# Performance work log

Measured on AMD Instinct MI355X. Metric: run time of the kernel, lower is better.

Reference implementation:

```python
import jax, jax.numpy as jnp
import numpy as np


def squash(s, axis=-1):
    sq = jnp.sum(s * s, axis=axis, keepdims=True)
    return sq / (1.0 + sq) * s / (jnp.sqrt(sq) + 1e-8)


def setup_inputs() -> dict:
    key = jax.random.key(0)
    k1, k2 = jax.random.split(key)
    B, IN_CAPS, IN_DIM = 32, 2048, 16
    NUM_CAPS, CAPS_DIM = 32, 32
    x = jax.random.normal(k1, (B, IN_CAPS, IN_DIM), dtype=jnp.float32)
    W = 0.01 * jax.random.normal(k2, (NUM_CAPS, IN_CAPS, CAPS_DIM, IN_DIM), dtype=jnp.float32)
    return {"x": x, "W": W, "routing_steps": 3}


def reference(x, W, routing_steps):
    # u_hat[b, j, i, c] = W[j, i, c, d] @ x[b, i, d]
    u_hat = jnp.einsum('jicd,bid->bjic', W, x)
    du = jax.lax.stop_gradient(u_hat)  # routing uses detached predictions
    B, J, I, C = u_hat.shape
    b = jnp.zeros((B, J, I, 1), dtype=u_hat.dtype)
    for _ in range(routing_steps - 1):
        c = jax.nn.softmax(b, axis=1)                  # over output capsules j
        s = jnp.sum(c * du, axis=2)                    # [B, J, C]
        v = squash(s)
        b = b + jnp.einsum('bjic,bjc->bji', du, v)[..., None]
    c = jax.nn.softmax(b, axis=1)
    s = jnp.sum(c * u_hat, axis=2)
    v = squash(s)                                      # [B, J, C]
    return v
```

## Files before the change

kernel.cpp:

```cpp
#include <hip/hip_runtime.h>
#include <hip/hip_bf16.h>

#define B_SZ   32
#define I_CAPS 2048
#define J_CAPS 32
#define C_DIM  32
#define D_DIM  16

#define IT     8
#define TILES  8
#define SPLIT  32
#define ROW_STRIDE 40

__device__ inline unsigned short f2bf(float f) {
    union { __hip_bfloat16 h; unsigned short u; } cv;
    cv.h = __float2bfloat16(f);
    return cv.u;
}
__device__ inline float bf2f(unsigned int u16) {
    unsigned int x = (u16 & 0xffffu) << 16;
    union { unsigned int u; float f; } cv; cv.u = x;
    return cv.f;
}

__global__ __launch_bounds__(256) void uhat_kernel(const float* __restrict__ W,
                                                   const float* __restrict__ x,
                                                   unsigned short* __restrict__ u) {
    const int i = blockIdx.x;
    const int t = threadIdx.x;

    __shared__ float xs[B_SZ][D_DIM];
    if (t < 128) {
        const int b = t >> 2, k = t & 3;
        const float4 v = *reinterpret_cast<const float4*>(
            &x[((size_t)b * I_CAPS + i) * D_DIM + k * 4]);
        *reinterpret_cast<float4*>(&xs[b][k * 4]) = v;
    }
    __syncthreads();

    const int j  = t >> 3;
    const int c0 = (t & 7) * 4;

    const float* Wp = W + (((size_t)j * I_CAPS + i) * C_DIM + c0) * D_DIM;
    float4 w[4][4];
#pragma unroll
    for (int k = 0; k < 4; ++k)
#pragma unroll
        for (int d4 = 0; d4 < 4; ++d4)
            w[k][d4] = *reinterpret_cast<const float4*>(Wp + k * D_DIM + d4 * 4);

#pragma unroll 2
    for (int b = 0; b < B_SZ; ++b) {
        float a0 = 0.f, a1 = 0.f, a2 = 0.f, a3 = 0.f;
#pragma unroll
        for (int d4 = 0; d4 < 4; ++d4) {
            const float4 xv = *reinterpret_cast<const float4*>(&xs[b][d4 * 4]);
            a0 += w[0][d4].x * xv.x + w[0][d4].y * xv.y + w[0][d4].z * xv.z + w[0][d4].w * xv.w;
            a1 += w[1][d4].x * xv.x + w[1][d4].y * xv.y + w[1][d4].z * xv.z + w[1][d4].w * xv.w;
            a2 += w[2][d4].x * xv.x + w[2][d4].y * xv.y + w[2][d4].z * xv.z + w[2][d4].w * xv.w;
            a3 += w[3][d4].x * xv.x + w[3][d4].y * xv.y + w[3][d4].z * xv.z + w[3][d4].w * xv.w;
        }
        ushort4 o;
        o.x = f2bf(a0); o.y = f2bf(a1); o.z = f2bf(a2); o.w = f2bf(a3);
        *reinterpret_cast<ushort4*>(
            &u[(((size_t)b * I_CAPS + i) * J_CAPS + j) * C_DIM + c0]) = o;
    }
}

__global__ __launch_bounds__(256) void route_kernel(const unsigned short* __restrict__ u,
                                                    const float* __restrict__ V,
                                                    float* __restrict__ s) {
    const int b      = blockIdx.y;
    const int i_base = blockIdx.x * (IT * TILES);
    const int t      = threadIdx.x;

    __shared__ unsigned short us[IT * J_CAPS * ROW_STRIDE];
    __shared__ float Vs[J_CAPS * 33];
    __shared__ float cjs[IT * J_CAPS];

    for (int n = t; n < J_CAPS * C_DIM; n += 256) {
        const int j = n >> 5, c = n & 31;
        Vs[j * 33 + c] = V[((size_t)b * J_CAPS + j) * C_DIM + c];
    }

    const int jA = t & 31, iA = t >> 5;
    const int jB = t >> 3, c4 = (t & 7) * 4;

    float sacc0 = 0.f, sacc1 = 0.f, sacc2 = 0.f, sacc3 = 0.f;

    for (int tile = 0; tile < TILES; ++tile) {
        const int i0 = i_base + tile * IT;
        __syncthreads();

        {
            const uint4* gsrc = reinterpret_cast<const uint4*>(
                u + ((size_t)b * I_CAPS + i0) * J_CAPS * C_DIM);
#pragma unroll
            for (int k = 0; k < 4; ++k) {
                const int n  = t + k * 256;
                const int il = n >> 7, rem = n & 127, j = rem >> 2, q = rem & 3;
                *reinterpret_cast<uint4*>(
                    &us[(il * J_CAPS + j) * ROW_STRIDE + q * 8]) = gsrc[n];
            }
        }
        __syncthreads();

        {
            const unsigned short* row = &us[(iA * J_CAPS + jA) * ROW_STRIDE];
            float l = 0.f;
#pragma unroll
            for (int cq = 0; cq < 8; ++cq) {
                const uint2 pk = *reinterpret_cast<const uint2*>(row + cq * 4);
                const float* Vr = &Vs[jA * 33 + cq * 4];
                l += bf2f(pk.x) * Vr[0] + bf2f(pk.x >> 16) * Vr[1]
                   + bf2f(pk.y) * Vr[2] + bf2f(pk.y >> 16) * Vr[3];
            }
            float m = l;
#pragma unroll
            for (int msk = 16; msk >= 1; msk >>= 1) m = fmaxf(m, __shfl_xor(m, msk));
            const float e = __expf(l - m);
            float ssum = e;
#pragma unroll
            for (int msk = 16; msk >= 1; msk >>= 1) ssum += __shfl_xor(ssum, msk);
            cjs[iA * J_CAPS + jA] = e / ssum;
        }
        __syncthreads();

        {
#pragma unroll
            for (int il = 0; il < IT; ++il) {
                const float cj = cjs[il * J_CAPS + jB];
                const unsigned short* row = &us[(il * J_CAPS + jB) * ROW_STRIDE + c4];
                const uint2 pk = *reinterpret_cast<const uint2*>(row);
                sacc0 += cj * bf2f(pk.x);
                sacc1 += cj * bf2f(pk.x >> 16);
                sacc2 += cj * bf2f(pk.y);
                sacc3 += cj * bf2f(pk.y >> 16);
            }
        }
    }

    float* sp = &s[((size_t)b * J_CAPS + jB) * C_DIM + c4];
    atomicAdd(sp + 0, sacc0);
    atomicAdd(sp + 1, sacc1);
    atomicAdd(sp + 2, sacc2);
    atomicAdd(sp + 3, sacc3);
}

__global__ __launch_bounds__(256) void squash_kernel(float* __restrict__ s,
                                                     float* __restrict__ V,
                                                     float* __restrict__ out,
                                                     int final_pass) {
    const int t   = threadIdx.x;
    const int row = blockIdx.x * 8 + (t >> 5);
    const int c   = t & 31;
    const float sv = s[row * 32 + c];
    float sq = sv * sv;
#pragma unroll
    for (int msk = 16; msk >= 1; msk >>= 1) sq += __shfl_xor(sq, msk);
    const float scale = sq / ((1.f + sq) * (sqrtf(sq) + 1e-8f));
    const float v = sv * scale;
    if (final_pass) out[row * 32 + c] = v;
    else            V[row * 32 + c] += v;
    s[row * 32 + c] = 0.f;
}

extern "C" void kernel_launch(void* const* d_in, const int* in_sizes, int n_in,
                              void* d_out, int out_size, void* d_ws, size_t ws_size,
                              hipStream_t stream) {
    const float* x = (const float*)d_in[0];
    const float* W = (const float*)d_in[1];
    float* out = (float*)d_out;

    unsigned short* u = (unsigned short*)d_ws;
    float* s = (float*)((char*)d_ws + (size_t)B_SZ * I_CAPS * J_CAPS * C_DIM * 2);
    float* V = s + B_SZ * J_CAPS * C_DIM;

    hipMemsetAsync(s, 0, 2 * (size_t)B_SZ * J_CAPS * C_DIM * sizeof(float), stream);

    uhat_kernel<<<I_CAPS, 256, 0, stream>>>(W, x, u);

    for (int p = 0; p < 3; ++p) {
        route_kernel<<<dim3(SPLIT, B_SZ), 256, 0, stream>>>(u, V, s);
        squash_kernel<<<(B_SZ * J_CAPS * C_DIM) / 256, 256, 0, stream>>>(s, V, out, p == 2 ? 1 : 0);
    }
}
```

Measured before the change: 193.7 us.

## Compute u_hat projection with fp16 MFMA instructions instead of scalar FMAs

Replaces the scalar FP32 u_hat kernel with a matrix-core version. W and x are converted to fp16 and fed to 16x16x32 MFMA, with the unused half of K zero-padded, and each block now handles two input capsules. The aim is to cut the ALU cost of the einsum, but the kernel is probably bound by reading W (128MB in fp32), so the gain may be small. It adds fp16 rounding of the inputs and wastes half of each MFMA on the zero padding. Its global access pattern also differs: each lane loads a 16-byte piece of a W row.

```diff
diff --git a/kernel.cpp b/kernel.cpp
--- a/kernel.cpp
+++ b/kernel.cpp
@@ -12,6 +12,9 @@
 #define SPLIT  32
 #define ROW_STRIDE 40
 
+typedef _Float16 f16x8 __attribute__((ext_vector_type(8)));
+typedef float    f32x4 __attribute__((ext_vector_type(4)));
+
 __device__ inline unsigned short f2bf(float f) {
     union { __hip_bfloat16 h; unsigned short u; } cv;
     cv.h = __float2bfloat16(f);
@@ -23,47 +26,59 @@
     return cv.f;
 }
 
-__global__ __launch_bounds__(256) void uhat_kernel(const float* __restrict__ W,
-                                                   const float* __restrict__ x,
-                                                   unsigned short* __restrict__ u) {
-    const int i = blockIdx.x;
-    const int t = threadIdx.x;
-
-    __shared__ float xs[B_SZ][D_DIM];
-    if (t < 128) {
-        const int b = t >> 2, k = t & 3;
-        const float4 v = *reinterpret_cast<const float4*>(
-            &x[((size_t)b * I_CAPS + i) * D_DIM + k * 4]);
-        *reinterpret_cast<float4*>(&xs[b][k * 4]) = v;
-    }
-    __syncthreads();
-
-    const int j  = t >> 3;
-    const int c0 = (t & 7) * 4;
-
-    const float* Wp = W + (((size_t)j * I_CAPS + i) * C_DIM + c0) * D_DIM;
-    float4 w[4][4];
-#pragma unroll
-    for (int k = 0; k < 4; ++k)
-#pragma unroll
-        for (int d4 = 0; d4 < 4; ++d4)
-            w[k][d4] = *reinterpret_cast<const float4*>(Wp + k * D_DIM + d4 * 4);
-
-#pragma unroll 2
-    for (int b = 0; b < B_SZ; ++b) {
-        float a0 = 0.f, a1 = 0.f, a2 = 0.f, a3 = 0.f;
-#pragma unroll
-        for (int d4 = 0; d4 < 4; ++d4) {
-            const float4 xv = *reinterpret_cast<const float4*>(&xs[b][d4 * 4]);
-            a0 += w[0][d4].x * xv.x + w[0][d4].y * xv.y + w[0][d4].z * xv.z + w[0][d4].w * xv.w;
-            a1 += w[1][d4].x * xv.x + w[1][d4].y * xv.y + w[1][d4].z * xv.z + w[1][d4].w * xv.w;
-            a2 += w[2][d4].x * xv.x + w[2][d4].y * xv.y + w[2][d4].z * xv.z + w[2][d4].w * xv.w;
-            a3 += w[3][d4].x * xv.x + w[3][d4].y * xv.y + w[3][d4].z * xv.z + w[3][d4].w * xv.w;
-        }
-        ushort4 o;
-        o.x = f2bf(a0); o.y = f2bf(a1); o.z = f2bf(a2); o.w = f2bf(a3);
-        *reinterpret_cast<ushort4*>(
-            &u[(((size_t)b * I_CAPS + i) * J_CAPS + j) * C_DIM + c0]) = o;
+#define IPB 2
+__global__ __launch_bounds__(256) void uhat_mfma(const float* __restrict__ W,
+                                                 const float* __restrict__ x,
+                                                 unsigned short* __restrict__ u) {
+    const int t    = threadIdx.x;
+    const int wave = t >> 6;
+    const int lane = t & 63;
+    const int lm   = lane & 15;
+    const int lq   = lane >> 4;
+
+    const int i0 = blockIdx.x * IPB;
+
+    for (int ii = 0; ii < IPB; ++ii) {
+        const int i = i0 + ii;
+
+        f16x8 bfr[2];
+#pragma unroll
+        for (int nt = 0; nt < 2; ++nt) {
+            const int b = nt * 16 + lm;
+            const float4 xv = *reinterpret_cast<const float4*>(
+                &x[((size_t)b * I_CAPS + i) * D_DIM + lq * 4]);
+            f16x8 f = {};
+            f[0] = (_Float16)xv.x; f[1] = (_Float16)xv.y;
+            f[2] = (_Float16)xv.z; f[3] = (_Float16)xv.w;
+            bfr[nt] = f;
+        }
+
+#pragma unroll 4
+        for (int k = 0; k < 16; ++k) {
+            const int mt = wave * 16 + k;
+            const int j  = mt >> 1;
+            const int c  = (mt & 1) * 16 + lm;
+            const float4 wv = *reinterpret_cast<const float4*>(
+                &W[(((size_t)j * I_CAPS + i) * C_DIM + c) * D_DIM + lq * 4]);
+            f16x8 a = {};
+            a[0] = (_Float16)wv.x; a[1] = (_Float16)wv.y;
+            a[2] = (_Float16)wv.z; a[3] = (_Float16)wv.w;
+
+            const f32x4 z = {0.f, 0.f, 0.f, 0.f};
+            f32x4 d0 = __builtin_amdgcn_mfma_f32_16x16x32_f16(a, bfr[0], z, 0, 0, 0);
+            f32x4 d1 = __builtin_amdgcn_mfma_f32_16x16x32_f16(a, bfr[1], z, 0, 0, 0);
+
+            const int m0 = mt * 16 + lq * 4;
+#pragma unroll
+            for (int nt = 0; nt < 2; ++nt) {
+                const f32x4 d = nt ? d1 : d0;
+                ushort4 o;
+                o.x = f2bf(d[0]); o.y = f2bf(d[1]); o.z = f2bf(d[2]); o.w = f2bf(d[3]);
+                const int b = nt * 16 + lm;
+                *reinterpret_cast<ushort4*>(
+                    &u[((size_t)b * I_CAPS + i) * (J_CAPS * C_DIM) + m0]) = o;
+            }
+        }
     }
 }
 
@@ -178,7 +193,7 @@
 
     hipMemsetAsync(s, 0, 2 * (size_t)B_SZ * J_CAPS * C_DIM * sizeof(float), stream);
 
-    uhat_kernel<<<I_CAPS, 256, 0, stream>>>(W, x, u);
+    uhat_mfma<<<I_CAPS / IPB, 256, 0, stream>>>(W, x, u);
 
     for (int p = 0; p < 3; ++p) {
         route_kernel<<<dim3(SPLIT, B_SZ), 256, 0, stream>>>(u, V, s);
```

New measurement: 204.8 us. 5.8% more time.
